# Kernel optimization log

Measured on AMD Instinct MI355X. Metric: run time of the kernel, lower is better.

## Reference

```python
import jax, jax.numpy as jnp
import numpy as np

B, N, K = 2, 1280, 48
C_NODE, C_EDGE, C_OUT = 384, 128, 128
C_BIAS = C_NODE // 2          # 192 (node_dilation=2)
HID = 2 * C_BIAS + C_EDGE     # 512
LN_EPS = 1e-5


def setup_inputs() -> dict:
    key = jax.random.key(0)
    ks = jax.random.split(key, 13)
    w = lambda k, shape: (jax.random.normal(k, shape, jnp.float32) * 0.02)
    return {
        "node_emb": jax.random.normal(ks[0], (B, N, C_NODE), jnp.float32),
        "edge_emb": jax.random.normal(ks[1], (B, N, K, C_EDGE), jnp.float32),
        "E_idx": jax.random.randint(ks[2], (B, N, K), 0, N),
        "Wi": w(ks[3], (C_NODE, C_BIAS)), "bi": jnp.zeros((C_BIAS,), jnp.float32),
        "W1": w(ks[4], (HID, HID)), "b1": jnp.zeros((HID,), jnp.float32),
        "W2": w(ks[5], (HID, HID)), "b2": jnp.zeros((HID,), jnp.float32),
        "Wf": w(ks[6], (HID, C_OUT)), "bf": jnp.zeros((C_OUT,), jnp.float32),
        "gamma": jnp.ones((C_OUT,), jnp.float32),
        "beta": jnp.zeros((C_OUT,), jnp.float32),
    }


def reference(node_emb, edge_emb, E_idx, Wi, bi, W1, b1, W2, b2, Wf, bf, gamma, beta):
    # initial_embed: [B, N, C_NODE] -> [B, N, C_BIAS]
    n = node_emb @ Wi + bi
    # edge_bias[b,i,k] = concat(n[b,i], n[b, E_idx[b,i,k]])  (tile + gather_edges fused)
    nbr = jax.vmap(lambda v, e: v[e])(n, E_idx)                     # [B, N, K, C_BIAS]
    slf = jnp.broadcast_to(n[:, :, None, :], nbr.shape)             # [B, N, K, C_BIAS]
    x = jnp.concatenate([edge_emb, slf, nbr], axis=-1)              # [B, N, K, HID]
    h = jax.nn.relu(x @ W1 + b1)
    h = jax.nn.relu(h @ W2 + b2)
    # final_layer on residual sum, then LayerNorm
    y = (h + x) @ Wf + bf                                           # [B, N, K, C_OUT]
    mu = jnp.mean(y, axis=-1, keepdims=True)
    var = jnp.mean((y - mu) ** 2, axis=-1, keepdims=True)
    return (y - mu) * jax.lax.rsqrt(var + LN_EPS) * gamma + beta
```

## Files before the change

kernel.cpp:

```cpp
#include <hip/hip_runtime.h>
#include <stdint.h>

#define BB    2
#define NN    1280
#define KK    48
#define CN    384
#define CE    128
#define CB    192
#define HID   512
#define CO    128
#define MM    (BB*NN*KK)
#define CH    (MM/2)

typedef __bf16 bf16x8 __attribute__((ext_vector_type(8)));
typedef float  f32x4  __attribute__((ext_vector_type(4)));
typedef unsigned short u16x8 __attribute__((ext_vector_type(8)));

__device__ __forceinline__ unsigned short f2bf(float f) {
  unsigned int i = __builtin_bit_cast(unsigned int, f);
  unsigned int r = (i + 0x7fffu + ((i >> 16) & 1u)) >> 16;
  return (unsigned short)r;
}
__device__ __forceinline__ float bf2f(unsigned short u) {
  unsigned int v = ((unsigned int)u) << 16;
  return __builtin_bit_cast(float, v);
}

__device__ __forceinline__ void gload_lds16(const void* g, void* l) {
  __builtin_amdgcn_global_load_lds(
      (const __attribute__((address_space(1))) void*)g,
      (__attribute__((address_space(3))) void*)l, 16, 0, 0);
}

__global__ void k_transpose_cast(const float* __restrict__ in,
                                 unsigned short* __restrict__ out,
                                 int R, int C) {
  __shared__ float tile[32][33];
  const int c0 = blockIdx.x * 32, r0 = blockIdx.y * 32;
  const int tx = threadIdx.x, ty = threadIdx.y;
#pragma unroll
  for (int dy = 0; dy < 32; dy += 8)
    tile[ty + dy][tx] = in[(size_t)(r0 + ty + dy) * C + c0 + tx];
  __syncthreads();
#pragma unroll
  for (int dy = 0; dy < 32; dy += 8)
    out[(size_t)(c0 + ty + dy) * R + r0 + tx] = f2bf(tile[tx][ty + dy]);
}

__global__ void k_node(const float* __restrict__ node,
                       const float* __restrict__ Wi,
                       const float* __restrict__ bi,
                       unsigned short* __restrict__ nbuf) {
  __shared__ float row[CN];
  const int blk = blockIdx.x;
  const float* src = node + (size_t)blk * CN;
  for (int c = threadIdx.x; c < CN; c += CB) row[c] = src[c];
  __syncthreads();
  const int t = threadIdx.x;
  float acc = bi[t];
#pragma unroll 8
  for (int c = 0; c < CN; ++c) acc += row[c] * Wi[(size_t)c * CB + t];
  nbuf[(size_t)blk * CB + t] = f2bf(acc);
}

__global__ void k_build_x(const float* __restrict__ edge,
                          const unsigned short* __restrict__ nbuf,
                          const int* __restrict__ eidx,
                          unsigned short* __restrict__ x) {
  const int w = threadIdx.x >> 6;
  const int l = threadIdx.x & 63;
  const int m = blockIdx.x * 4 + w;
  const int bi = m / KK;
  uint4 val;
  if (l < 16) {
    const float4* e4 = (const float4*)(edge + (size_t)m * CE);
    float4 a = e4[l * 2], b = e4[l * 2 + 1];
    u16x8 p;
    p[0] = f2bf(a.x); p[1] = f2bf(a.y); p[2] = f2bf(a.z); p[3] = f2bf(a.w);
    p[4] = f2bf(b.x); p[5] = f2bf(b.y); p[6] = f2bf(b.z); p[7] = f2bf(b.w);
    val = __builtin_bit_cast(uint4, p);
  } else if (l < 40) {
    val = ((const uint4*)(nbuf + (size_t)bi * CB))[l - 16];
  } else {
    const int b = bi / NN;
    const int e = eidx[m];
    val = ((const uint4*)(nbuf + (size_t)(b * NN + e) * CB))[l - 40];
  }
  ((uint4*)(x + (size_t)m * HID))[l] = val;
}

template <int ADD_X>
__global__ __launch_bounds__(256, 2)
void k_gemm(const unsigned short* __restrict__ A,
            const unsigned short* __restrict__ Wt,
            const float* __restrict__ bias,
            const unsigned short* xres,
            unsigned short* out) {
  __shared__ char lds[32768];
  char* ldsA = lds;
  char* ldsB = lds + 16384;
  const int flat = blockIdx.x;
  const int xcd = flat & 7;
  const int p = flat >> 3;
  const int m0 = (xcd * 60 + (p >> 2)) * 128;
  const int n0 = (p & 3) * 128;
  const int tid = threadIdx.x;
  const int l = tid & 63;
  const int w = tid >> 6;
  const int wm = w >> 1, wn = w & 1;
  const int sr = l >> 3;
  const int pc = l & 7;

  f32x4 acc[4][4];
#pragma unroll
  for (int i = 0; i < 4; ++i)
#pragma unroll
    for (int j = 0; j < 4; ++j) acc[i][j] = (f32x4){0.f, 0.f, 0.f, 0.f};

  for (int k0 = 0; k0 < HID; k0 += 64) {
    __syncthreads();
#pragma unroll
    for (int ii = 0; ii < 4; ++ii) {
      const int i = w * 4 + ii;
      const int r = i * 8 + sr;
      const int lc = pc ^ sr;
      gload_lds16(A  + (size_t)(m0 + r) * HID + k0 + lc * 8, ldsA + i * 1024);
      gload_lds16(Wt + (size_t)(n0 + r) * HID + k0 + lc * 8, ldsB + i * 1024);
    }
    __syncthreads();
#pragma unroll
    for (int kk = 0; kk < 2; ++kk) {
      bf16x8 av[4], bv[4];
#pragma unroll
      for (int t = 0; t < 4; ++t) {
        const int ra = wm * 64 + t * 16 + (l & 15);
        const int ca = (kk * 4 + (l >> 4)) ^ (ra & 7);
        av[t] = *(const bf16x8*)(ldsA + ra * 128 + ca * 16);
        const int rb = wn * 64 + t * 16 + (l & 15);
        const int cb = (kk * 4 + (l >> 4)) ^ (rb & 7);
        bv[t] = *(const bf16x8*)(ldsB + rb * 128 + cb * 16);
      }
#pragma unroll
      for (int mt = 0; mt < 4; ++mt)
#pragma unroll
        for (int nt = 0; nt < 4; ++nt)
          acc[mt][nt] = __builtin_amdgcn_mfma_f32_16x16x32_bf16(av[mt], bv[nt], acc[mt][nt], 0, 0, 0);
    }
  }

  __syncthreads();
  unsigned short* tile = (unsigned short*)lds;
  const int q = l >> 4, cc = l & 15;
#pragma unroll
  for (int nt = 0; nt < 4; ++nt) {
    const int col = wn * 64 + nt * 16 + cc;
    const float bvv = bias[n0 + col];
    const int cn = col >> 3, cb = col & 7;
#pragma unroll
    for (int mt = 0; mt < 4; ++mt) {
      const int r0_ = wm * 64 + mt * 16 + q * 4;
#pragma unroll
      for (int r = 0; r < 4; ++r) {
        float v = acc[mt][nt][r] + bvv;
        v = v > 0.f ? v : 0.f;
        const int row = r0_ + r;
        tile[row * 128 + ((cn ^ (row & 7)) << 3) + cb] = f2bf(v);
      }
    }
  }
  __syncthreads();
#pragma unroll
  for (int i = 0; i < 8; ++i) {
    const int c = i * 256 + tid;
    const int row = c >> 4, cn = c & 15;
    u16x8 vv = *(const u16x8*)(tile + row * 128 + ((cn ^ (row & 7)) << 3));
    const size_t goff = (size_t)(m0 + row) * HID + n0 + cn * 8;
    if (ADD_X) {
      u16x8 xv = *(const u16x8*)(xres + goff);
#pragma unroll
      for (int j = 0; j < 8; ++j) vv[j] = f2bf(bf2f(vv[j]) + bf2f(xv[j]));
    }
    *(u16x8*)(out + goff) = vv;
  }
}

__global__ __launch_bounds__(256, 2)
void k_final(const unsigned short* __restrict__ A,
             const unsigned short* __restrict__ Wft,
             const float* __restrict__ bias,
             const float* __restrict__ gamma,
             const float* __restrict__ beta,
             float* __restrict__ out) {
  __shared__ char lds[32768];
  char* ldsA = lds;
  char* ldsB = lds + 16384;
  const int m0 = blockIdx.x * 128;
  const int tid = threadIdx.x;
  const int l = tid & 63;
  const int w = tid >> 6;
  const int sr = l >> 3, pc = l & 7;

  f32x4 acc[2][8];
#pragma unroll
  for (int i = 0; i < 2; ++i)
#pragma unroll
    for (int j = 0; j < 8; ++j) acc[i][j] = (f32x4){0.f, 0.f, 0.f, 0.f};

  for (int k0 = 0; k0 < HID; k0 += 64) {
    __syncthreads();
#pragma unroll
    for (int ii = 0; ii < 4; ++ii) {
      const int i = w * 4 + ii;
      const int r = i * 8 + sr;
      const int lc = pc ^ sr;
      gload_lds16(A   + (size_t)(m0 + r) * HID + k0 + lc * 8, ldsA + i * 1024);
      gload_lds16(Wft + (size_t)r * HID + k0 + lc * 8,        ldsB + i * 1024);
    }
    __syncthreads();
#pragma unroll
    for (int kk = 0; kk < 2; ++kk) {
      bf16x8 av[2], bv[8];
#pragma unroll
      for (int t = 0; t < 2; ++t) {
        const int ra = w * 32 + t * 16 + (l & 15);
        const int ca = (kk * 4 + (l >> 4)) ^ (ra & 7);
        av[t] = *(const bf16x8*)(ldsA + ra * 128 + ca * 16);
      }
#pragma unroll
      for (int t = 0; t < 8; ++t) {
        const int rb = t * 16 + (l & 15);
        const int cb = (kk * 4 + (l >> 4)) ^ (rb & 7);
        bv[t] = *(const bf16x8*)(ldsB + rb * 128 + cb * 16);
      }
#pragma unroll
      for (int mt = 0; mt < 2; ++mt)
#pragma unroll
        for (int nt = 0; nt < 8; ++nt)
          acc[mt][nt] = __builtin_amdgcn_mfma_f32_16x16x32_bf16(av[mt], bv[nt], acc[mt][nt], 0, 0, 0);
    }
  }

  const int q = l >> 4, cc = l & 15;
  float gg[8], bb[8], bs[8];
#pragma unroll
  for (int j = 0; j < 8; ++j) {
    const int col = j * 16 + cc;
    gg[j] = gamma[col];
    bb[j] = beta[col];
    bs[j] = bias[col];
  }
#pragma unroll
  for (int mt = 0; mt < 2; ++mt) {
#pragma unroll
    for (int r = 0; r < 4; ++r) {
      float s = 0.f, ss = 0.f;
#pragma unroll
      for (int j = 0; j < 8; ++j) {
        const float v = acc[mt][j][r] + bs[j];
        acc[mt][j][r] = v;
        s += v;
        ss += v * v;
      }
#pragma unroll
      for (int mk = 1; mk < 16; mk <<= 1) {
        s  += __shfl_xor(s, mk, 64);
        ss += __shfl_xor(ss, mk, 64);
      }
      const float mu = s * (1.f / 128.f);
      const float var = ss * (1.f / 128.f) - mu * mu;
      const float rstd = rsqrtf(var + 1e-5f);
      const int row = m0 + w * 32 + mt * 16 + q * 4 + r;
#pragma unroll
      for (int j = 0; j < 8; ++j) {
        const float v = (acc[mt][j][r] - mu) * rstd * gg[j] + bb[j];
        out[(size_t)row * CO + j * 16 + cc] = v;
      }
    }
  }
}

#define O_N    ((size_t)0)
#define O_WT1  ((size_t)0x100000)
#define O_WT2  (O_WT1 + (size_t)0x80000)
#define O_WFT  (O_WT2 + (size_t)0x80000)
#define O_X    ((size_t)0x300000)
#define O_H1   (O_X + (size_t)MM * HID * 2)

extern "C" void kernel_launch(void* const* d_in, const int* in_sizes, int n_in,
                              void* d_out, int out_size, void* d_ws, size_t ws_size,
                              hipStream_t stream) {
  const float* node  = (const float*)d_in[0];
  const float* edge  = (const float*)d_in[1];
  const int*   eidx  = (const int*)d_in[2];
  const float* Wi    = (const float*)d_in[3];
  const float* bi    = (const float*)d_in[4];
  const float* W1    = (const float*)d_in[5];
  const float* b1    = (const float*)d_in[6];
  const float* W2    = (const float*)d_in[7];
  const float* b2    = (const float*)d_in[8];
  const float* Wf    = (const float*)d_in[9];
  const float* bfv   = (const float*)d_in[10];
  const float* gamma = (const float*)d_in[11];
  const float* beta  = (const float*)d_in[12];
  float* out = (float*)d_out;

  char* ws = (char*)d_ws;
  unsigned short* nbuf = (unsigned short*)(ws + O_N);
  unsigned short* Wt1  = (unsigned short*)(ws + O_WT1);
  unsigned short* Wt2  = (unsigned short*)(ws + O_WT2);
  unsigned short* Wft  = (unsigned short*)(ws + O_WFT);
  unsigned short* xbuf = (unsigned short*)(ws + O_X);
  unsigned short* h1   = (unsigned short*)(ws + O_H1);

  k_transpose_cast<<<dim3(HID / 32, HID / 32), dim3(32, 8), 0, stream>>>(W1, Wt1, HID, HID);
  k_transpose_cast<<<dim3(HID / 32, HID / 32), dim3(32, 8), 0, stream>>>(W2, Wt2, HID, HID);
  k_transpose_cast<<<dim3(CO / 32, HID / 32), dim3(32, 8), 0, stream>>>(Wf, Wft, HID, CO);

  k_node<<<BB * NN, CB, 0, stream>>>(node, Wi, bi, nbuf);

  k_build_x<<<MM / 4, 256, 0, stream>>>(edge, nbuf, eidx, xbuf);

  for (int c = 0; c < 2; ++c) {
    unsigned short* xc = xbuf + (size_t)c * CH * HID;
    k_gemm<0><<<(CH / 128) * 4, 256, 0, stream>>>(xc, Wt1, b1, nullptr, h1);
    k_gemm<1><<<(CH / 128) * 4, 256, 0, stream>>>(h1, Wt2, b2, xc, xc);
  }

  k_final<<<MM / 128, 256, 0, stream>>>(xbuf, Wft, bfv, gamma, beta, out);
}
```

Baseline: 415.7 us.

## Fuse edge-feature concat gather into first GEMM and residual epilogue

Removes the separate build_x pass that materialised the full bf16 concatenated input. The first GEMM now builds its A tiles directly from fp32 edge features (converted in registers) and from gathered node-embedding rows via global_load_lds. The second GEMM's epilogue recomputes the residual x from edge, nbuf and eidx instead of reading a stored copy. The final layer is launched per half using a half-sized buffer, and the K loops are fully unrolled. This saves a full write and read of x, at the cost of uncoalesced gather loads inside the GEMM main loop and more register pressure.

```diff
diff --git a/kernel.cpp b/kernel.cpp
--- a/kernel.cpp
+++ b/kernel.cpp
@@ -32,6 +32,29 @@
       (__attribute__((address_space(3))) void*)l, 16, 0, 0);
 }
 
+__device__ __forceinline__ void mfma_tiles(const char* ldsA, const char* ldsB,
+                                           int l, int wm, int wn,
+                                           f32x4 (&acc)[4][4]) {
+#pragma unroll
+  for (int kk = 0; kk < 2; ++kk) {
+    bf16x8 av[4], bv[4];
+#pragma unroll
+    for (int t = 0; t < 4; ++t) {
+      const int ra = wm * 64 + t * 16 + (l & 15);
+      const int ca = (kk * 4 + (l >> 4)) ^ (ra & 7);
+      av[t] = *(const bf16x8*)(ldsA + ra * 128 + ca * 16);
+      const int rb = wn * 64 + t * 16 + (l & 15);
+      const int cb = (kk * 4 + (l >> 4)) ^ (rb & 7);
+      bv[t] = *(const bf16x8*)(ldsB + rb * 128 + cb * 16);
+    }
+#pragma unroll
+    for (int mt = 0; mt < 4; ++mt)
+#pragma unroll
+      for (int nt = 0; nt < 4; ++nt)
+        acc[mt][nt] = __builtin_amdgcn_mfma_f32_16x16x32_bf16(av[mt], bv[nt], acc[mt][nt], 0, 0, 0);
+  }
+}
+
 __global__ void k_transpose_cast(const float* __restrict__ in,
                                  unsigned short* __restrict__ out,
                                  int R, int C) {
@@ -63,39 +86,14 @@
   nbuf[(size_t)blk * CB + t] = f2bf(acc);
 }
 
-__global__ void k_build_x(const float* __restrict__ edge,
-                          const unsigned short* __restrict__ nbuf,
-                          const int* __restrict__ eidx,
-                          unsigned short* __restrict__ x) {
-  const int w = threadIdx.x >> 6;
-  const int l = threadIdx.x & 63;
-  const int m = blockIdx.x * 4 + w;
-  const int bi = m / KK;
-  uint4 val;
-  if (l < 16) {
-    const float4* e4 = (const float4*)(edge + (size_t)m * CE);
-    float4 a = e4[l * 2], b = e4[l * 2 + 1];
-    u16x8 p;
-    p[0] = f2bf(a.x); p[1] = f2bf(a.y); p[2] = f2bf(a.z); p[3] = f2bf(a.w);
-    p[4] = f2bf(b.x); p[5] = f2bf(b.y); p[6] = f2bf(b.z); p[7] = f2bf(b.w);
-    val = __builtin_bit_cast(uint4, p);
-  } else if (l < 40) {
-    val = ((const uint4*)(nbuf + (size_t)bi * CB))[l - 16];
-  } else {
-    const int b = bi / NN;
-    const int e = eidx[m];
-    val = ((const uint4*)(nbuf + (size_t)(b * NN + e) * CB))[l - 40];
-  }
-  ((uint4*)(x + (size_t)m * HID))[l] = val;
-}
-
-template <int ADD_X>
 __global__ __launch_bounds__(256, 2)
-void k_gemm(const unsigned short* __restrict__ A,
-            const unsigned short* __restrict__ Wt,
-            const float* __restrict__ bias,
-            const unsigned short* xres,
-            unsigned short* out) {
+void k_gemm1(const float* __restrict__ edge,
+             const unsigned short* __restrict__ nbuf,
+             const int* __restrict__ eidx,
+             const unsigned short* __restrict__ Wt,
+             const float* __restrict__ bias,
+             unsigned short* __restrict__ out,
+             int mbase, int b) {
   __shared__ char lds[32768];
   char* ldsA = lds;
   char* ldsB = lds + 16384;
@@ -108,8 +106,20 @@
   const int l = tid & 63;
   const int w = tid >> 6;
   const int wm = w >> 1, wn = w & 1;
-  const int sr = l >> 3;
-  const int pc = l & 7;
+  const int sr = l >> 3, pc = l & 7;
+  const int lc = pc ^ sr;
+
+  int rr[4], big[4], nbrg[4];
+  size_t mg[4];
+#pragma unroll
+  for (int ii = 0; ii < 4; ++ii) {
+    const int r = (w * 4 + ii) * 8 + sr;
+    rr[ii] = r;
+    const int m = mbase + m0 + r;
+    mg[ii] = (size_t)m;
+    big[ii] = m / KK;
+    nbrg[ii] = b * NN + eidx[m];
+  }
 
   f32x4 acc[4][4];
 #pragma unroll
@@ -117,35 +127,35 @@
 #pragma unroll
     for (int j = 0; j < 4; ++j) acc[i][j] = (f32x4){0.f, 0.f, 0.f, 0.f};
 
+#pragma unroll
   for (int k0 = 0; k0 < HID; k0 += 64) {
+    uint4 rga[4];
+    if (k0 < 128) {
+#pragma unroll
+      for (int ii = 0; ii < 4; ++ii) {
+        const float4* ep = (const float4*)(edge + mg[ii] * CE + k0 + lc * 8);
+        float4 x0 = ep[0], x1 = ep[1];
+        u16x8 pk;
+        pk[0] = f2bf(x0.x); pk[1] = f2bf(x0.y); pk[2] = f2bf(x0.z); pk[3] = f2bf(x0.w);
+        pk[4] = f2bf(x1.x); pk[5] = f2bf(x1.y); pk[6] = f2bf(x1.z); pk[7] = f2bf(x1.w);
+        rga[ii] = __builtin_bit_cast(uint4, pk);
+      }
+    }
     __syncthreads();
 #pragma unroll
     for (int ii = 0; ii < 4; ++ii) {
       const int i = w * 4 + ii;
-      const int r = i * 8 + sr;
-      const int lc = pc ^ sr;
-      gload_lds16(A  + (size_t)(m0 + r) * HID + k0 + lc * 8, ldsA + i * 1024);
-      gload_lds16(Wt + (size_t)(n0 + r) * HID + k0 + lc * 8, ldsB + i * 1024);
-    }
-    __syncthreads();
-#pragma unroll
-    for (int kk = 0; kk < 2; ++kk) {
-      bf16x8 av[4], bv[4];
-#pragma unroll
-      for (int t = 0; t < 4; ++t) {
-        const int ra = wm * 64 + t * 16 + (l & 15);
-        const int ca = (kk * 4 + (l >> 4)) ^ (ra & 7);
-        av[t] = *(const bf16x8*)(ldsA + ra * 128 + ca * 16);
-        const int rb = wn * 64 + t * 16 + (l & 15);
-        const int cb = (kk * 4 + (l >> 4)) ^ (rb & 7);
-        bv[t] = *(const bf16x8*)(ldsB + rb * 128 + cb * 16);
-      }
-#pragma unroll
-      for (int mt = 0; mt < 4; ++mt)
-#pragma unroll
-        for (int nt = 0; nt < 4; ++nt)
-          acc[mt][nt] = __builtin_amdgcn_mfma_f32_16x16x32_bf16(av[mt], bv[nt], acc[mt][nt], 0, 0, 0);
-    }
+      gload_lds16(Wt + (size_t)(n0 + rr[ii]) * HID + k0 + lc * 8, ldsB + i * 1024);
+      if (k0 < 128) {
+        *(uint4*)(ldsA + i * 1024 + l * 16) = rga[ii];
+      } else if (k0 < 320) {
+        gload_lds16(nbuf + (size_t)big[ii] * CB + (k0 - 128) + lc * 8, ldsA + i * 1024);
+      } else {
+        gload_lds16(nbuf + (size_t)nbrg[ii] * CB + (k0 - 320) + lc * 8, ldsA + i * 1024);
+      }
+    }
+    __syncthreads();
+    mfma_tiles(ldsA, ldsB, l, wm, wn, acc);
   }
 
   __syncthreads();
@@ -174,13 +184,110 @@
     const int c = i * 256 + tid;
     const int row = c >> 4, cn = c & 15;
     u16x8 vv = *(const u16x8*)(tile + row * 128 + ((cn ^ (row & 7)) << 3));
-    const size_t goff = (size_t)(m0 + row) * HID + n0 + cn * 8;
-    if (ADD_X) {
-      u16x8 xv = *(const u16x8*)(xres + goff);
-#pragma unroll
-      for (int j = 0; j < 8; ++j) vv[j] = f2bf(bf2f(vv[j]) + bf2f(xv[j]));
-    }
-    *(u16x8*)(out + goff) = vv;
+    *(u16x8*)(out + (size_t)(m0 + row) * HID + n0 + cn * 8) = vv;
+  }
+}
+
+__global__ __launch_bounds__(256, 2)
+void k_gemm2(const unsigned short* __restrict__ A,
+             const unsigned short* __restrict__ Wt,
+             const float* __restrict__ bias,
+             const float* __restrict__ edge,
+             const unsigned short* __restrict__ nbuf,
+             const int* __restrict__ eidx,
+             unsigned short* __restrict__ out,
+             int mbase, int b) {
+  __shared__ char lds[32768];
+  char* ldsA = lds;
+  char* ldsB = lds + 16384;
+  const int flat = blockIdx.x;
+  const int xcd = flat & 7;
+  const int p = flat >> 3;
+  const int m0 = (xcd * 60 + (p >> 2)) * 128;
+  const int n0 = (p & 3) * 128;
+  const int tid = threadIdx.x;
+  const int l = tid & 63;
+  const int w = tid >> 6;
+  const int wm = w >> 1, wn = w & 1;
+  const int sr = l >> 3, pc = l & 7;
+  const int lc = pc ^ sr;
+
+  f32x4 acc[4][4];
+#pragma unroll
+  for (int i = 0; i < 4; ++i)
+#pragma unroll
+    for (int j = 0; j < 4; ++j) acc[i][j] = (f32x4){0.f, 0.f, 0.f, 0.f};
+
+#pragma unroll
+  for (int k0 = 0; k0 < HID; k0 += 64) {
+    __syncthreads();
+#pragma unroll
+    for (int ii = 0; ii < 4; ++ii) {
+      const int i = w * 4 + ii;
+      const int r = i * 8 + sr;
+      gload_lds16(A  + (size_t)(m0 + r) * HID + k0 + lc * 8, ldsA + i * 1024);
+      gload_lds16(Wt + (size_t)(n0 + r) * HID + k0 + lc * 8, ldsB + i * 1024);
+    }
+    __syncthreads();
+    mfma_tiles(ldsA, ldsB, l, wm, wn, acc);
+  }
+
+  __syncthreads();
+  unsigned short* tile = (unsigned short*)lds;
+  const int q = l >> 4, cc = l & 15;
+#pragma unroll
+  for (int nt = 0; nt < 4; ++nt) {
+    const int col = wn * 64 + nt * 16 + cc;
+    const float bvv = bias[n0 + col];
+    const int cn = col >> 3, cb = col & 7;
+#pragma unroll
+    for (int mt = 0; mt < 4; ++mt) {
+      const int r0_ = wm * 64 + mt * 16 + q * 4;
+#pragma unroll
+      for (int r = 0; r < 4; ++r) {
+        float v = acc[mt][nt][r] + bvv;
+        v = v > 0.f ? v : 0.f;
+        const int row = r0_ + r;
+        tile[row * 128 + ((cn ^ (row & 7)) << 3) + cb] = f2bf(v);
+      }
+    }
+  }
+  __syncthreads();
+#pragma unroll
+  for (int i = 0; i < 8; ++i) {
+    const int c = i * 256 + tid;
+    const int row = c >> 4, cn = c & 15;
+    u16x8 vv = *(const u16x8*)(tile + row * 128 + ((cn ^ (row & 7)) << 3));
+    const int m = mbase + m0 + row;
+    float rv[8];
+    if (n0 == 0) {
+      const float4* ep = (const float4*)(edge + (size_t)m * CE + cn * 8);
+      float4 x0 = ep[0], x1 = ep[1];
+      rv[0] = x0.x; rv[1] = x0.y; rv[2] = x0.z; rv[3] = x0.w;
+      rv[4] = x1.x; rv[5] = x1.y; rv[6] = x1.z; rv[7] = x1.w;
+    } else if (n0 == 128) {
+      u16x8 xv = *(const u16x8*)(nbuf + (size_t)(m / KK) * CB + cn * 8);
+#pragma unroll
+      for (int j = 0; j < 8; ++j) rv[j] = bf2f(xv[j]);
+    } else if (n0 == 256) {
+      u16x8 xv;
+      if (cn < 8) {
+        xv = *(const u16x8*)(nbuf + (size_t)(m / KK) * CB + 128 + cn * 8);
+      } else {
+        const int e = eidx[m];
+        xv = *(const u16x8*)(nbuf + (size_t)(b * NN + e) * CB + cn * 8 - 64);
+      }
+#pragma unroll
+      for (int j = 0; j < 8; ++j) rv[j] = bf2f(xv[j]);
+    } else {
+      const int e = eidx[m];
+      u16x8 xv = *(const u16x8*)(nbuf + (size_t)(b * NN + e) * CB + 64 + cn * 8);
+#pragma unroll
+      for (int j = 0; j < 8; ++j) rv[j] = bf2f(xv[j]);
+    }
+#pragma unroll
+    for (int j = 0; j < 8; ++j) vv[j] = f2bf(bf2f(vv[j]) + rv[j]);
+    *(u16x8*)(out + (size_t)(m0 + row) * HID + n0 + cn * 8) = vv;
   }
 }
 
@@ -199,6 +306,7 @@
   const int l = tid & 63;
   const int w = tid >> 6;
   const int sr = l >> 3, pc = l & 7;
+  const int lc = pc ^ sr;
 
   f32x4 acc[2][8];
 #pragma unroll
@@ -206,13 +314,13 @@
 #pragma unroll
     for (int j = 0; j < 8; ++j) acc[i][j] = (f32x4){0.f, 0.f, 0.f, 0.f};
 
+#pragma unroll
   for (int k0 = 0; k0 < HID; k0 += 64) {
     __syncthreads();
 #pragma unroll
     for (int ii = 0; ii < 4; ++ii) {
       const int i = w * 4 + ii;
       const int r = i * 8 + sr;
-      const int lc = pc ^ sr;
       gload_lds16(A   + (size_t)(m0 + r) * HID + k0 + lc * 8, ldsA + i * 1024);
       gload_lds16(Wft + (size_t)r * HID + k0 + lc * 8,        ldsB + i * 1024);
     }
@@ -283,8 +391,8 @@
 #define O_WT1  ((size_t)0x100000)
 #define O_WT2  (O_WT1 + (size_t)0x80000)
 #define O_WFT  (O_WT2 + (size_t)0x80000)
-#define O_X    ((size_t)0x300000)
-#define O_H1   (O_X + (size_t)MM * HID * 2)
+#define O_H1   ((size_t)0x300000)
+#define O_A    (O_H1 + (size_t)CH * HID * 2)
 
 extern "C" void kernel_launch(void* const* d_in, const int* in_sizes, int n_in,
                               void* d_out, int out_size, void* d_ws, size_t ws_size,
@@ -309,8 +417,8 @@
   unsigned short* Wt1  = (unsigned short*)(ws + O_WT1);
   unsigned short* Wt2  = (unsigned short*)(ws + O_WT2);
   unsigned short* Wft  = (unsigned short*)(ws + O_WFT);
-  unsigned short* xbuf = (unsigned short*)(ws + O_X);
   unsigned short* h1   = (unsigned short*)(ws + O_H1);
+  unsigned short* abuf = (unsigned short*)(ws + O_A);
 
   k_transpose_cast<<<dim3(HID / 32, HID / 32), dim3(32, 8), 0, stream>>>(W1, Wt1, HID, HID);
   k_transpose_cast<<<dim3(HID / 32, HID / 32), dim3(32, 8), 0, stream>>>(W2, Wt2, HID, HID);
@@ -318,13 +426,9 @@
 
   k_node<<<BB * NN, CB, 0, stream>>>(node, Wi, bi, nbuf);
 
-  k_build_x<<<MM / 4, 256, 0, stream>>>(edge, nbuf, eidx, xbuf);
-
   for (int c = 0; c < 2; ++c) {
-    unsigned short* xc = xbuf + (size_t)c * CH * HID;
-    k_gemm<0><<<(CH / 128) * 4, 256, 0, stream>>>(xc, Wt1, b1, nullptr, h1);
-    k_gemm<1><<<(CH / 128) * 4, 256, 0, stream>>>(h1, Wt2, b2, xc, xc);
-  }
-
-  k_final<<<MM / 128, 256, 0, stream>>>(xbuf, Wft, bfv, gamma, beta, out);
-}
+    k_gemm1<<<(CH / 128) * 4, 256, 0, stream>>>(edge, nbuf, eidx, Wt1, b1, h1, c * CH, c);
+    k_gemm2<<<(CH / 128) * 4, 256, 0, stream>>>(h1, Wt2, b2, edge, nbuf, eidx, abuf, c * CH, c);
+    k_final<<<CH / 128, 256, 0, stream>>>(abuf, Wft, bfv, gamma, beta, out + (size_t)c * CH * CO);
+  }
+}
```

Result: faster. 386.0 us (-7.2%).
